# Optimization experiments

Measured on AMD Instinct MI355X. Metric: run time of the kernel, lower is better.

Reference implementation:

```python
import jax, jax.numpy as jnp
import numpy as np
from jax import lax

B, NP = 4, 8192          # events, points per event (equal-sized batches)
RATIO, R, K = 0.25, 0.2, 64
MP = int(NP * RATIO)     # sampled centers per event
D_IN = 32
BIG = 1e10


def _fps_one(pos):
    # Farthest point sampling (deterministic start at index 0). pos: [NP,3] -> [MP] int32
    d = jnp.sum((pos - pos[0]) ** 2, axis=-1)
    sel = jnp.zeros((MP,), jnp.int32)

    def body(i, carry):
        sel, d = carry
        nxt = jnp.argmax(d).astype(jnp.int32)
        sel = sel.at[i].set(nxt)
        d = jnp.minimum(d, jnp.sum((pos - pos[nxt]) ** 2, axis=-1))
        return sel, d

    sel, _ = lax.fori_loop(1, MP, body, (sel, d))
    return sel


def _ball_query_one(centers, pos):
    # centers: [MP,3], pos: [NP,3] -> neighbor idx [MP,K] int32, validity mask [MP,K]
    d2 = jnp.sum((centers[:, None, :] - pos[None, :, :]) ** 2, axis=-1)  # [MP,NP]
    d2m = jnp.where(d2 <= R * R, d2, BIG)
    neg, idx = lax.top_k(-d2m, K)          # K nearest within radius (deterministic)
    mask = (-neg) <= R * R
    return idx.astype(jnp.int32), mask


def reference(x, pos, batch, W1, b1, W2, b2, W3, b3):
    xb = x.reshape(B, NP, D_IN)
    pb = pos.reshape(B, NP, 3)

    sel = jax.vmap(_fps_one)(pb)                                   # [B,MP]
    centers = jnp.take_along_axis(pb, sel[..., None], axis=1)      # [B,MP,3]
    idx, mask = jax.vmap(_ball_query_one)(centers, pb)             # [B,MP,K]

    gather = jax.vmap(lambda a, i: a[i])
    pos_j = gather(pb, idx)                                        # [B,MP,K,3]
    x_j = gather(xb, idx)                                          # [B,MP,K,D_IN]

    rel = pos_j - centers[:, :, None, :]
    h = jnp.concatenate([x_j, rel], axis=-1)                       # [B,MP,K,D_IN+3]
    h = jax.nn.relu(h @ W1 + b1)
    h = jax.nn.relu(h @ W2 + b2)
    h = jax.nn.relu(h @ W3 + b3)                                   # [B,MP,K,128]

    h = jnp.where(mask[..., None], h, -BIG)
    x_out = jnp.max(h, axis=2).reshape(B * MP, -1)                 # max aggregation
    pos_out = centers.reshape(B * MP, 3)
    batch_out = jnp.repeat(jnp.arange(B, dtype=jnp.int32), MP)
    return x_out, pos_out, batch_out


def setup_inputs() -> dict:
    key = jax.random.key(0)
    ks = jax.random.split(key, 8)
    x = jax.random.normal(ks[0], (B * NP, D_IN), jnp.float32)
    pos = jax.random.uniform(ks[1], (B * NP, 3), jnp.float32)
    batch = (jnp.arange(B * NP) // NP).astype(jnp.int64)
    W1 = jax.random.normal(ks[2], (D_IN + 3, 64), jnp.float32) * 0.05
    b1 = jnp.zeros((64,), jnp.float32)
    W2 = jax.random.normal(ks[3], (64, 64), jnp.float32) * 0.05
    b2 = jnp.zeros((64,), jnp.float32)
    W3 = jax.random.normal(ks[4], (64, 128), jnp.float32) * 0.05
    b3 = jnp.zeros((128,), jnp.float32)
    return {"x": x, "pos": pos, "batch": batch, "W1": W1, "b1": b1,
            "W2": W2, "b2": b2, "W3": W3, "b3": b3}
```

## Files before the change

kernel.cpp:

```cpp
#include <hip/hip_runtime.h>


#define BATCH 4
#define NP 8192
#define MP 2048
#define KNN 64
#define DIN 32

__device__ __forceinline__ float fmax_nc(float a, float b) {
  float r;
  asm("v_max_f32 %0, %1, %2" : "=v"(r) : "v"(a), "v"(b));
  return r;
}

#define DPP_FMAX(v, ctrl)                                                     \
  {                                                                           \
    int _t = __builtin_amdgcn_update_dpp(__float_as_int(v),                   \
                                         __float_as_int(v), (ctrl), 0xF,      \
                                         0xF, false);                         \
    (v) = fmax_nc((v), __int_as_float(_t));                                   \
  }

#define DPP_MINU(v, ctrl)                                                     \
  {                                                                           \
    unsigned _t = (unsigned)__builtin_amdgcn_update_dpp((int)(v), (int)(v),   \
                                                        (ctrl), 0xF, 0xF,    \
                                                        false);               \
    (v) = ((v) < _t) ? (v) : _t;                                              \
  }

typedef float v2f __attribute__((ext_vector_type(2)));

__device__ __forceinline__ v2f d2_pair(v2f ppx, v2f ppy, v2f ppz,
                                       v2f cxn, v2f cyn, v2f czn) {
  v2f t, dx, dy, dz;
  asm("v_pk_add_f32 %1, %4, %7\n\t"
      "v_pk_add_f32 %2, %5, %8\n\t"
      "v_pk_add_f32 %3, %6, %9\n\t"
      "v_pk_mul_f32 %0, %2, %2\n\t"
      "v_pk_fma_f32 %0, %1, %1, %0\n\t"
      "v_pk_fma_f32 %0, %3, %3, %0"
      : "=&v"(t), "=&v"(dx), "=&v"(dy), "=&v"(dz)
      : "v"(ppx), "v"(ppy), "v"(ppz), "v"(cxn), "v"(cyn), "v"(czn));
  return t;
}

__global__ __launch_bounds__(1024) void fps_k(const float* __restrict__ pos,
                                              const float* __restrict__ x,
                                              const float* __restrict__ W1,
                                              const float* __restrict__ W2,
                                              const float* __restrict__ W3,
                                              float* __restrict__ pout,
                                              float* __restrict__ bout,
                                              float* __restrict__ P1,
                                              float* __restrict__ W2T,
                                              float* __restrict__ W3T)
{
  const int bid = blockIdx.x;
  const int tid = threadIdx.x;

  if (bid >= BATCH) {
    if (bid < BATCH + 2048) {
      const int j = (bid - BATCH) * 16 + (tid >> 6);
      const int c = tid & 63;
      const float* __restrict__ xr = x + (size_t)j * DIN;
      float acc = 0.f;
#pragma unroll
      for (int k = 0; k < DIN; k++) acc += xr[k] * W1[k * 64 + c];
      P1[(size_t)j * 64 + c] = acc;
    } else {
#pragma unroll
      for (int it = 0; it < 12; it++) {
        const int e = it * 1024 + tid;
        if (e < 64 * 64) {
          const int c = e >> 6, k = e & 63;
          W2T[e] = W2[k * 64 + c];
        } else {
          const int e2 = e - 64 * 64;
          const int c = e2 >> 6, k = e2 & 63;
          W3T[e2] = W3[k * 128 + c];
        }
      }
    }
    return;
  }

  const int b = bid;
  const int lane = tid & 63, wid = tid >> 6;
  const float* __restrict__ pb = pos + (size_t)b * NP * 3;
  const int base = tid * 8;

  bout[b * MP + tid] = (float)b;
  bout[b * MP + 1024 + tid] = (float)b;

  __shared__ __align__(16) float sc[2][16][4];

  float t[24];
  const float4* __restrict__ pv = (const float4*)(pb + (size_t)tid * 24);
#pragma unroll
  for (int q = 0; q < 6; q++) *(float4*)&t[q * 4] = pv[q];

  v2f px[4], py[4], pz[4], d[4];
#pragma unroll
  for (int j = 0; j < 4; j++) {
    px[j].x = t[6 * j + 0]; py[j].x = t[6 * j + 1]; pz[j].x = t[6 * j + 2];
    px[j].y = t[6 * j + 3]; py[j].y = t[6 * j + 4]; pz[j].y = t[6 * j + 5];
  }

  const float c0x = pb[0], c0y = pb[1], c0z = pb[2];
  if (tid == 0) {
    pout[(size_t)b * MP * 3 + 0] = c0x;
    pout[(size_t)b * MP * 3 + 1] = c0y;
    pout[(size_t)b * MP * 3 + 2] = c0z;
  }

  float bv = -1.f;
  {
    const v2f cxn = {-c0x, -c0x}, cyn = {-c0y, -c0y}, czn = {-c0z, -c0z};
#pragma unroll
    for (int j = 0; j < 4; j++) {
      const v2f nd = d2_pair(px[j], py[j], pz[j], cxn, cyn, czn);
      d[j] = nd;
      bv = fmaxf(fmaxf(nd.x, nd.y), bv);
    }
  }

  for (int i = 1; i < MP; i++) {
    float v = bv;
    DPP_FMAX(v, 0x111);
    DPP_FMAX(v, 0x112);
    DPP_FMAX(v, 0x114);
    DPP_FMAX(v, 0x118);
    DPP_FMAX(v, 0x142);
    DPP_FMAX(v, 0x143);
    const float wmax =
        __int_as_float(__builtin_amdgcn_readlane(__float_as_int(v), 63));

    const unsigned long long m = __ballot(bv == wmax);
    const int src = (int)__builtin_ctzll(m);
    const int p = i & 1;
    if (lane == src) {
      float ox = px[3].y, oy = py[3].y, oz = pz[3].y;
#pragma unroll
      for (int k = 6; k >= 0; k--) {
        const float dv = (k & 1) ? d[k >> 1].y : d[k >> 1].x;
        if (dv == wmax) {
          ox = (k & 1) ? px[k >> 1].y : px[k >> 1].x;
          oy = (k & 1) ? py[k >> 1].y : py[k >> 1].x;
          oz = (k & 1) ? pz[k >> 1].y : pz[k >> 1].x;
        }
      }
      float4 q; q.x = ox; q.y = oy; q.z = oz; q.w = wmax;
      *(float4*)&sc[p][wid][0] = q;
    }
    __syncthreads();

    const float4 q = *(const float4*)&sc[p][lane & 15][0];
    const float v2 = q.w;
    float v2r = v2;
    DPP_FMAX(v2r, 0x111);
    DPP_FMAX(v2r, 0x112);
    DPP_FMAX(v2r, 0x114);
    DPP_FMAX(v2r, 0x118);
    const float mv =
        __int_as_float(__builtin_amdgcn_readlane(__float_as_int(v2r), 15));
    const unsigned long long m2 = __ballot(v2 == mv);
    const int mw = (int)__builtin_ctzll(m2);
    const float ncx =
        __int_as_float(__builtin_amdgcn_readlane(__float_as_int(q.x), mw));
    const float ncy =
        __int_as_float(__builtin_amdgcn_readlane(__float_as_int(q.y), mw));
    const float ncz =
        __int_as_float(__builtin_amdgcn_readlane(__float_as_int(q.z), mw));

    if (tid == 0) {
      pout[((size_t)b * MP + i) * 3 + 0] = ncx;
      pout[((size_t)b * MP + i) * 3 + 1] = ncy;
      pout[((size_t)b * MP + i) * 3 + 2] = ncz;
    }

    const v2f cxn = {-ncx, -ncx}, cyn = {-ncy, -ncy}, czn = {-ncz, -ncz};
    bv = -1.f;
#pragma unroll
    for (int j = 0; j < 4; j++) {
      const v2f nd = d2_pair(px[j], py[j], pz[j], cxn, cyn, czn);
      v2f dn;
      dn.x = fminf(d[j].x, nd.x);
      dn.y = fminf(d[j].y, nd.y);
      d[j] = dn;
      bv = fmaxf(fmaxf(dn.x, dn.y), bv);
    }
  }
}

__global__ __launch_bounds__(64) void ballq_k(const float* __restrict__ pos,
                                              const float* __restrict__ pout,
                                              int* __restrict__ nbr)
{
  const int wg = blockIdx.x;
  const int lane = threadIdx.x;
  const int b = wg >> 11;
  const float* __restrict__ pb = pos + (size_t)b * NP * 3;
  const float cx = pout[(size_t)wg * 3 + 0];
  const float cy = pout[(size_t)wg * 3 + 1];
  const float cz = pout[(size_t)wg * 3 + 2];
  const float R2 = (float)(0.2 * 0.2);

  __shared__ unsigned long long cand[1024];
  int cnt = 0;
  for (int basej = 0; basej < NP; basej += 64) {
    const int j = basej + lane;
    float dx = pb[j * 3 + 0] - cx;
    float dy = pb[j * 3 + 1] - cy;
    float dz = pb[j * 3 + 2] - cz;
    float d2 = dx * dx + dy * dy + dz * dz;
    bool in = (d2 <= R2);
    unsigned long long mb = __ballot(in);
    int pre = (int)__popcll(mb & ((1ull << lane) - 1ull));
    int slot = cnt + pre;
    if (in && slot < 1024)
      cand[slot] = ((unsigned long long)__float_as_uint(d2) << 32) | (unsigned int)j;
    cnt += (int)__popcll(mb);
  }
  if (cnt > 1024) cnt = 1024;

  unsigned long long last = 0;
  int myout = -1;
  for (int r = 0; r < KNN; r++) {
    unsigned long long v = ~0ull;
    for (int s = lane; s < cnt; s += 64) {
      const unsigned long long c = cand[s];
      if (c >= last && c < v) v = c;
    }
    const unsigned hi = (unsigned)(v >> 32);
    unsigned h = hi;
    DPP_MINU(h, 0x111);
    DPP_MINU(h, 0x112);
    DPP_MINU(h, 0x114);
    DPP_MINU(h, 0x118);
    DPP_MINU(h, 0x142);
    DPP_MINU(h, 0x143);
    const unsigned mhi = (unsigned)__builtin_amdgcn_readlane((int)h, 63);
    const unsigned lo = (hi == mhi) ? (unsigned)v : 0xffffffffu;
    unsigned l2 = lo;
    DPP_MINU(l2, 0x111);
    DPP_MINU(l2, 0x112);
    DPP_MINU(l2, 0x114);
    DPP_MINU(l2, 0x118);
    DPP_MINU(l2, 0x142);
    DPP_MINU(l2, 0x143);
    const unsigned mlo = (unsigned)__builtin_amdgcn_readlane((int)l2, 63);

    if (lane == r) myout = (mhi == 0xffffffffu) ? -1 : (int)mlo;
    last = (mhi == 0xffffffffu)
               ? ~0ull
               : ((((unsigned long long)mhi << 32) | mlo) + 1ull);
  }
  nbr[(size_t)wg * KNN + lane] = myout;
}

__global__ __launch_bounds__(64) void mlp_k(const float* __restrict__ pos,
    const float* __restrict__ P1, const float* __restrict__ W1,
    const float* __restrict__ b1, const float* __restrict__ W2T,
    const float* __restrict__ b2, const float* __restrict__ W3T,
    const float* __restrict__ b3, const int* __restrict__ nbr,
    const float* __restrict__ pout, float* __restrict__ xout)
{
  __shared__ __align__(16) float h2s[64 * 68];
  const int wg = blockIdx.x;
  const int lane = threadIdx.x;
  const int b = wg >> 11;
  const int idx = nbr[(size_t)wg * KNN + lane];
  const bool valid = idx >= 0;
  const int j = valid ? idx : 0;
  const float cx = pout[(size_t)wg * 3 + 0];
  const float cy = pout[(size_t)wg * 3 + 1];
  const float cz = pout[(size_t)wg * 3 + 2];
  const float* __restrict__ pj = pos + ((size_t)b * NP + j) * 3;
  const float rx = pj[0] - cx, ry = pj[1] - cy, rz = pj[2] - cz;
  const float* __restrict__ p1r =
      (const float*)__builtin_assume_aligned(P1 + ((size_t)b * NP + j) * 64, 16);

  float h1[64];
#pragma unroll
  for (int k = 0; k < 64; k++) {
    float v = p1r[k] + rx * W1[32 * 64 + k] + ry * W1[33 * 64 + k]
                     + rz * W1[34 * 64 + k] + b1[k];
    h1[k] = fmaxf(v, 0.f);
  }

  for (int c4 = 0; c4 < 16; c4++) {
    float a0 = b2[c4 * 4 + 0], a1 = b2[c4 * 4 + 1];
    float a2 = b2[c4 * 4 + 2], a3 = b2[c4 * 4 + 3];
    const float* __restrict__ w0 = W2T + (c4 * 4 + 0) * 64;
    const float* __restrict__ w1 = W2T + (c4 * 4 + 1) * 64;
    const float* __restrict__ w2 = W2T + (c4 * 4 + 2) * 64;
    const float* __restrict__ w3 = W2T + (c4 * 4 + 3) * 64;
#pragma unroll
    for (int k = 0; k < 64; k++) {
      a0 += h1[k] * w0[k]; a1 += h1[k] * w1[k];
      a2 += h1[k] * w2[k]; a3 += h1[k] * w3[k];
    }
    float4 q;
    q.x = fmaxf(a0, 0.f); q.y = fmaxf(a1, 0.f);
    q.z = fmaxf(a2, 0.f); q.w = fmaxf(a3, 0.f);
    *(float4*)&h2s[lane * 68 + c4 * 4] = q;
  }

  float4 keep = make_float4(0.f, 0.f, 0.f, 0.f);
  const float* __restrict__ h2p = &h2s[lane * 68];
  for (int c4 = 0; c4 < 32; c4++) {
    float a0 = b3[c4 * 4 + 0], a1 = b3[c4 * 4 + 1];
    float a2 = b3[c4 * 4 + 2], a3 = b3[c4 * 4 + 3];
    const float* __restrict__ w0 = W3T + (c4 * 4 + 0) * 64;
    const float* __restrict__ w1 = W3T + (c4 * 4 + 1) * 64;
    const float* __restrict__ w2 = W3T + (c4 * 4 + 2) * 64;
    const float* __restrict__ w3 = W3T + (c4 * 4 + 3) * 64;
#pragma unroll
    for (int k4 = 0; k4 < 16; k4++) {
      float4 h = *(const float4*)&h2p[k4 * 4];
      a0 += h.x * w0[k4 * 4 + 0]; a0 += h.y * w0[k4 * 4 + 1];
      a0 += h.z * w0[k4 * 4 + 2]; a0 += h.w * w0[k4 * 4 + 3];
      a1 += h.x * w1[k4 * 4 + 0]; a1 += h.y * w1[k4 * 4 + 1];
      a1 += h.z * w1[k4 * 4 + 2]; a1 += h.w * w1[k4 * 4 + 3];
      a2 += h.x * w2[k4 * 4 + 0]; a2 += h.y * w2[k4 * 4 + 1];
      a2 += h.z * w2[k4 * 4 + 2]; a2 += h.w * w2[k4 * 4 + 3];
      a3 += h.x * w3[k4 * 4 + 0]; a3 += h.y * w3[k4 * 4 + 1];
      a3 += h.z * w3[k4 * 4 + 2]; a3 += h.w * w3[k4 * 4 + 3];
    }
    a0 = valid ? fmaxf(a0, 0.f) : 0.f;
    a1 = valid ? fmaxf(a1, 0.f) : 0.f;
    a2 = valid ? fmaxf(a2, 0.f) : 0.f;
    a3 = valid ? fmaxf(a3, 0.f) : 0.f;
#pragma unroll
    for (int off = 1; off < 64; off <<= 1) {
      a0 = fmaxf(a0, __shfl_xor(a0, off));
      a1 = fmaxf(a1, __shfl_xor(a1, off));
      a2 = fmaxf(a2, __shfl_xor(a2, off));
      a3 = fmaxf(a3, __shfl_xor(a3, off));
    }
    if (lane == c4) { keep.x = a0; keep.y = a1; keep.z = a2; keep.w = a3; }
  }
  if (lane < 32)
    *(float4*)&xout[(size_t)wg * 128 + lane * 4] = keep;
}

extern "C" void kernel_launch(void* const* d_in, const int* in_sizes, int n_in,
                              void* d_out, int out_size, void* d_ws, size_t ws_size,
                              hipStream_t stream)
{
  const float* x   = (const float*)d_in[0];
  const float* pos = (const float*)d_in[1];
  const float* W1 = (const float*)d_in[3];
  const float* b1 = (const float*)d_in[4];
  const float* W2 = (const float*)d_in[5];
  const float* b2 = (const float*)d_in[6];
  const float* W3 = (const float*)d_in[7];
  const float* b3 = (const float*)d_in[8];

  float* out  = (float*)d_out;
  float* xout = out;
  float* pout = out + 8192 * 128;
  float* bout = out + 8192 * 128 + 8192 * 3;

  char* ws = (char*)d_ws;
  float* P1  = (float*)ws;
  float* W2T = (float*)(ws + 8388608);
  float* W3T = (float*)(ws + 8404992);
  int*   nbr = (int*)(ws + 8437760);

  fps_k<<<dim3(BATCH + 2048 + 1), dim3(1024), 0, stream>>>(
      pos, x, W1, W2, W3, pout, bout, P1, W2T, W3T);
  ballq_k<<<dim3(BATCH * MP), dim3(64), 0, stream>>>(pos, pout, nbr);
  mlp_k<<<dim3(BATCH * MP), dim3(64), 0, stream>>>(pos, P1, W1, b1, W2T, b2,
                                                   W3T, b3, nbr, pout, xout);
}
```

Baseline: 2.779 ms.

## Shrink FPS blocks to 4 waves with 32 points per thread and LDS point table

The farthest-point-sampling block drops from 16 waves to 4 waves, with each thread holding 32 points instead of 8. This shortens the cross-wave reduction, which now covers 4 partial maxima instead of 16 and needs fewer DPP steps per iteration. The winner's coordinates are looked up by index from a 96 KB LDS copy of the event's points rather than gathered through readlanes. The trade is four times more per-thread distance work per iteration, plus larger register use and heavy LDS allocation at one block per CU. The hand-written packed asm and the helper blocks are also reworked to match the 256-thread geometry.

```diff
diff --git a/kernel.cpp b/kernel.cpp
--- a/kernel.cpp
+++ b/kernel.cpp
@@ -6,19 +6,14 @@
 #define MP 2048
 #define KNN 64
 #define DIN 32
-
-__device__ __forceinline__ float fmax_nc(float a, float b) {
-  float r;
-  asm("v_max_f32 %0, %1, %2" : "=v"(r) : "v"(a), "v"(b));
-  return r;
-}
+#define PPL 32
 
 #define DPP_FMAX(v, ctrl)                                                     \
   {                                                                           \
     int _t = __builtin_amdgcn_update_dpp(__float_as_int(v),                   \
                                          __float_as_int(v), (ctrl), 0xF,      \
                                          0xF, false);                         \
-    (v) = fmax_nc((v), __int_as_float(_t));                                   \
+    (v) = fmaxf((v), __int_as_float(_t));                                     \
   }
 
 #define DPP_MINU(v, ctrl)                                                     \
@@ -31,37 +26,23 @@
 
 typedef float v2f __attribute__((ext_vector_type(2)));
 
-__device__ __forceinline__ v2f d2_pair(v2f ppx, v2f ppy, v2f ppz,
-                                       v2f cxn, v2f cyn, v2f czn) {
-  v2f t, dx, dy, dz;
-  asm("v_pk_add_f32 %1, %4, %7\n\t"
-      "v_pk_add_f32 %2, %5, %8\n\t"
-      "v_pk_add_f32 %3, %6, %9\n\t"
-      "v_pk_mul_f32 %0, %2, %2\n\t"
-      "v_pk_fma_f32 %0, %1, %1, %0\n\t"
-      "v_pk_fma_f32 %0, %3, %3, %0"
-      : "=&v"(t), "=&v"(dx), "=&v"(dy), "=&v"(dz)
-      : "v"(ppx), "v"(ppy), "v"(ppz), "v"(cxn), "v"(cyn), "v"(czn));
-  return t;
-}
-
-__global__ __launch_bounds__(1024) void fps_k(const float* __restrict__ pos,
-                                              const float* __restrict__ x,
-                                              const float* __restrict__ W1,
-                                              const float* __restrict__ W2,
-                                              const float* __restrict__ W3,
-                                              float* __restrict__ pout,
-                                              float* __restrict__ bout,
-                                              float* __restrict__ P1,
-                                              float* __restrict__ W2T,
-                                              float* __restrict__ W3T)
+__global__ __launch_bounds__(256, 1) void fps_k(const float* __restrict__ pos,
+                                                const float* __restrict__ x,
+                                                const float* __restrict__ W1,
+                                                const float* __restrict__ W2,
+                                                const float* __restrict__ W3,
+                                                float* __restrict__ pout,
+                                                float* __restrict__ bout,
+                                                float* __restrict__ P1,
+                                                float* __restrict__ W2T,
+                                                float* __restrict__ W3T)
 {
   const int bid = blockIdx.x;
   const int tid = threadIdx.x;
 
   if (bid >= BATCH) {
-    if (bid < BATCH + 2048) {
-      const int j = (bid - BATCH) * 16 + (tid >> 6);
+    if (bid < BATCH + 8192) {
+      const int j = (bid - BATCH) * 4 + (tid >> 6);
       const int c = tid & 63;
       const float* __restrict__ xr = x + (size_t)j * DIN;
       float acc = 0.f;
@@ -69,17 +50,14 @@
       for (int k = 0; k < DIN; k++) acc += xr[k] * W1[k * 64 + c];
       P1[(size_t)j * 64 + c] = acc;
     } else {
-#pragma unroll
-      for (int it = 0; it < 12; it++) {
-        const int e = it * 1024 + tid;
-        if (e < 64 * 64) {
-          const int c = e >> 6, k = e & 63;
-          W2T[e] = W2[k * 64 + c];
-        } else {
-          const int e2 = e - 64 * 64;
-          const int c = e2 >> 6, k = e2 & 63;
-          W3T[e2] = W3[k * 128 + c];
-        }
+      const int e = (bid - (BATCH + 8192)) * 256 + tid;
+      if (e < 64 * 64) {
+        const int c = e >> 6, k = e & 63;
+        W2T[e] = W2[k * 64 + c];
+      } else {
+        const int e2 = e - 64 * 64;
+        const int c = e2 >> 6, k = e2 & 63;
+        W3T[e2] = W3[k * 128 + c];
       }
     }
     return;
@@ -88,23 +66,19 @@
   const int b = bid;
   const int lane = tid & 63, wid = tid >> 6;
   const float* __restrict__ pb = pos + (size_t)b * NP * 3;
-  const int base = tid * 8;
-
-  bout[b * MP + tid] = (float)b;
-  bout[b * MP + 1024 + tid] = (float)b;
-
-  __shared__ __align__(16) float sc[2][16][4];
-
-  float t[24];
-  const float4* __restrict__ pv = (const float4*)(pb + (size_t)tid * 24);
-#pragma unroll
-  for (int q = 0; q < 6; q++) *(float4*)&t[q * 4] = pv[q];
-
-  v2f px[4], py[4], pz[4], d[4];
-#pragma unroll
-  for (int j = 0; j < 4; j++) {
-    px[j].x = t[6 * j + 0]; py[j].x = t[6 * j + 1]; pz[j].x = t[6 * j + 2];
-    px[j].y = t[6 * j + 3]; py[j].y = t[6 * j + 4]; pz[j].y = t[6 * j + 5];
+  const int base = tid * PPL;
+
+#pragma unroll
+  for (int q = 0; q < 8; q++) bout[b * MP + q * 256 + tid] = (float)b;
+
+  __shared__ __align__(16) float ptab[NP * 3];
+  __shared__ unsigned long long slt[2][4];
+
+  {
+    float4* __restrict__ pt4 = (float4*)ptab;
+    const float4* __restrict__ pv4 = (const float4*)pb;
+#pragma unroll
+    for (int q = 0; q < 24; q++) pt4[q * 256 + tid] = pv4[q * 256 + tid];
   }
 
   const float c0x = pb[0], c0y = pb[1], c0z = pb[2];
@@ -113,13 +87,27 @@
     pout[(size_t)b * MP * 3 + 1] = c0y;
     pout[(size_t)b * MP * 3 + 2] = c0z;
   }
+  __syncthreads();
+
+  v2f px[16], py[16], pz[16], d[16];
+#pragma unroll
+  for (int j = 0; j < 16; j++) {
+    const float* __restrict__ pp = &ptab[tid * (PPL * 3) + j * 6];
+    const v2f A = *(const v2f*)&pp[0];
+    const v2f Bv = *(const v2f*)&pp[2];
+    const v2f C = *(const v2f*)&pp[4];
+    px[j].x = A.x;  px[j].y = Bv.y;
+    py[j].x = A.y;  py[j].y = C.x;
+    pz[j].x = Bv.x; pz[j].y = C.y;
+  }
 
   float bv = -1.f;
   {
-    const v2f cxn = {-c0x, -c0x}, cyn = {-c0y, -c0y}, czn = {-c0z, -c0z};
-#pragma unroll
-    for (int j = 0; j < 4; j++) {
-      const v2f nd = d2_pair(px[j], py[j], pz[j], cxn, cyn, czn);
+    const v2f cx = {c0x, c0x}, cy = {c0y, c0y}, cz = {c0z, c0z};
+#pragma unroll
+    for (int j = 0; j < 16; j++) {
+      v2f dx = px[j] - cx, dy = py[j] - cy, dz = pz[j] - cz;
+      v2f nd = dx * dx + dy * dy + dz * dz;
       d[j] = nd;
       bv = fmaxf(fmaxf(nd.x, nd.y), bv);
     }
@@ -140,38 +128,30 @@
     const int src = (int)__builtin_ctzll(m);
     const int p = i & 1;
     if (lane == src) {
-      float ox = px[3].y, oy = py[3].y, oz = pz[3].y;
-#pragma unroll
-      for (int k = 6; k >= 0; k--) {
+      int ks = PPL - 1;
+#pragma unroll
+      for (int k = PPL - 2; k >= 0; k--) {
         const float dv = (k & 1) ? d[k >> 1].y : d[k >> 1].x;
-        if (dv == wmax) {
-          ox = (k & 1) ? px[k >> 1].y : px[k >> 1].x;
-          oy = (k & 1) ? py[k >> 1].y : py[k >> 1].x;
-          oz = (k & 1) ? pz[k >> 1].y : pz[k >> 1].x;
-        }
+        if (dv == wmax) ks = k;
       }
-      float4 q; q.x = ox; q.y = oy; q.z = oz; q.w = wmax;
-      *(float4*)&sc[p][wid][0] = q;
+      slt[p][wid] = ((unsigned long long)__float_as_uint(wmax) << 32)
+                    | (unsigned)(base + ks);
     }
     __syncthreads();
 
-    const float4 q = *(const float4*)&sc[p][lane & 15][0];
-    const float v2 = q.w;
+    const unsigned long long kv = slt[p][lane & 3];
+    const float v2 = __uint_as_float((unsigned)(kv >> 32));
     float v2r = v2;
     DPP_FMAX(v2r, 0x111);
     DPP_FMAX(v2r, 0x112);
-    DPP_FMAX(v2r, 0x114);
-    DPP_FMAX(v2r, 0x118);
     const float mv =
-        __int_as_float(__builtin_amdgcn_readlane(__float_as_int(v2r), 15));
+        __int_as_float(__builtin_amdgcn_readlane(__float_as_int(v2r), 3));
     const unsigned long long m2 = __ballot(v2 == mv);
     const int mw = (int)__builtin_ctzll(m2);
-    const float ncx =
-        __int_as_float(__builtin_amdgcn_readlane(__float_as_int(q.x), mw));
-    const float ncy =
-        __int_as_float(__builtin_amdgcn_readlane(__float_as_int(q.y), mw));
-    const float ncz =
-        __int_as_float(__builtin_amdgcn_readlane(__float_as_int(q.z), mw));
+    const int js = __builtin_amdgcn_readlane((int)(unsigned)kv, mw);
+    const float ncx = ptab[js * 3 + 0];
+    const float ncy = ptab[js * 3 + 1];
+    const float ncz = ptab[js * 3 + 2];
 
     if (tid == 0) {
       pout[((size_t)b * MP + i) * 3 + 0] = ncx;
@@ -179,11 +159,12 @@
       pout[((size_t)b * MP + i) * 3 + 2] = ncz;
     }
 
-    const v2f cxn = {-ncx, -ncx}, cyn = {-ncy, -ncy}, czn = {-ncz, -ncz};
+    const v2f cx = {ncx, ncx}, cy = {ncy, ncy}, cz = {ncz, ncz};
     bv = -1.f;
 #pragma unroll
-    for (int j = 0; j < 4; j++) {
-      const v2f nd = d2_pair(px[j], py[j], pz[j], cxn, cyn, czn);
+    for (int j = 0; j < 16; j++) {
+      v2f dx = px[j] - cx, dy = py[j] - cy, dz = pz[j] - cz;
+      v2f nd = dx * dx + dy * dy + dz * dz;
       v2f dn;
       dn.x = fminf(d[j].x, nd.x);
       dn.y = fminf(d[j].y, nd.y);
@@ -369,7 +350,7 @@
   float* W3T = (float*)(ws + 8404992);
   int*   nbr = (int*)(ws + 8437760);
 
-  fps_k<<<dim3(BATCH + 2048 + 1), dim3(1024), 0, stream>>>(
+  fps_k<<<dim3(BATCH + 8192 + 48), dim3(256), 0, stream>>>(
       pos, x, W1, W2, W3, pout, bout, P1, W2T, W3T);
   ballq_k<<<dim3(BATCH * MP), dim3(64), 0, stream>>>(pos, pout, nbr);
   mlp_k<<<dim3(BATCH * MP), dim3(64), 0, stream>>>(pos, P1, W1, b1, W2T, b2,
```

Result: faster. 2.693 ms (-3.1%).
